# Kernel tuning notes

Hardware: AMD Instinct MI355X
Metric: run time of the kernel (lower is better)

Reference implementation:

```python
import jax, jax.numpy as jnp
import numpy as np

N, E, B, L = 20000, 320000, 64, 4
DIN_SEQ, DIN_STR, HID = 1280, 128, 256
NHEAD, HDIM = 8, 32
EPS = 1e-5
SLOPE = 0.2


def setup_inputs() -> dict:
    key = jax.random.key(0)
    ks = iter(jax.random.split(key, 64))
    def nrm(shape, scale=0.05):
        return jax.random.normal(next(ks), shape, dtype=jnp.float32) * scale
    return {
        "seq_x": jax.random.normal(next(ks), (N, DIN_SEQ), dtype=jnp.float32),
        "struct_x": jax.random.normal(next(ks), (N, DIN_STR), dtype=jnp.float32),
        "seq_edge_index": jax.random.randint(next(ks), (2, E), 0, N),
        "struct_edge_index": jax.random.randint(next(ks), (2, E), 0, N),
        "seq_batch": jnp.sort(jax.random.randint(next(ks), (N,), 0, B)),
        "struct_batch": jnp.sort(jax.random.randint(next(ks), (N,), 0, B)),
        "seq_proj_W": nrm((DIN_SEQ, HID)), "seq_proj_b": nrm((HID,)),
        "gcn_W": nrm((L, HID, HID)), "gcn_b": nrm((L, HID)),
        "seq_bn_g": jnp.ones((L, HID), jnp.float32), "seq_bn_b": jnp.zeros((L, HID), jnp.float32),
        "struct_proj_W": nrm((DIN_STR, HID)), "struct_proj_b": nrm((HID,)),
        "gat_W": nrm((L, HID, HID)), "gat_att_src": nrm((L, NHEAD, HDIM)),
        "gat_att_dst": nrm((L, NHEAD, HDIM)), "gat_b": nrm((L, HID)),
        "struct_bn_g": jnp.ones((L, HID), jnp.float32), "struct_bn_b": jnp.zeros((L, HID), jnp.float32),
        "Wq": nrm((HID, HID)), "bq": nrm((HID,)),
        "Wk": nrm((HID, HID)), "bk": nrm((HID,)),
        "Wv": nrm((HID, HID)), "bv": nrm((HID,)),
        "Wo": nrm((HID, HID)), "bo": nrm((HID,)),
        "fus_W": nrm((2 * HID, HID)), "fus_b": nrm((HID,)),
        "p1_W": nrm((HID, HID // 2)), "p1_b": nrm((HID // 2,)),
        "p2_W": nrm((HID // 2, 1)), "p2_b": nrm((1,)),
    }


def _add_self_loops(edge_index, n):
    loops = jnp.arange(n, dtype=edge_index.dtype)
    return jnp.concatenate([edge_index[0], loops]), jnp.concatenate([edge_index[1], loops])


def _batchnorm(x, g, b):
    # PyG BatchNorm forward (training-mode batch stats, biased variance, eps=1e-5)
    mu = x.mean(axis=0)
    var = x.var(axis=0)
    return g * (x - mu) * jax.lax.rsqrt(var + EPS) + b


def _gcn(x, src, dst, W, b):
    # GCNConv: symmetric-normalized gather -> scatter-add, self loops already appended
    n = x.shape[0]
    deg = jax.ops.segment_sum(jnp.ones_like(src, dtype=x.dtype), dst, num_segments=n)
    dinv = jax.lax.rsqrt(jnp.maximum(deg, 1.0))
    h = x @ W
    msg = h[src] * (dinv[src] * dinv[dst])[:, None]
    return jax.ops.segment_sum(msg, dst, num_segments=n) + b


def _seg_softmax(e, dst, n):
    m = jax.ops.segment_max(e, dst, num_segments=n)
    ex = jnp.exp(e - m[dst])
    s = jax.ops.segment_sum(ex, dst, num_segments=n)
    return ex / s[dst]


def _gat(x, src, dst, W, a_src, a_dst, b):
    # GATConv: per-edge LeakyReLU attention, softmax over incoming edges, concat heads
    n = x.shape[0]
    h = (x @ W).reshape(n, NHEAD, HDIM)
    e = jax.nn.leaky_relu((h * a_src).sum(-1)[src] + (h * a_dst).sum(-1)[dst], SLOPE)  # [E,H]
    alpha = _seg_softmax(e, dst, n)
    out = jax.ops.segment_sum(h[src] * alpha[:, :, None], dst, num_segments=n)
    return out.reshape(n, NHEAD * HDIM) + b


def _mean_pool(x, batch, nb):
    s = jax.ops.segment_sum(x, batch, num_segments=nb)
    c = jax.ops.segment_sum(jnp.ones((x.shape[0],), x.dtype), batch, num_segments=nb)
    return s / jnp.maximum(c, 1.0)[:, None]


def reference(seq_x, struct_x, seq_edge_index, struct_edge_index, seq_batch, struct_batch,
              seq_proj_W, seq_proj_b, gcn_W, gcn_b, seq_bn_g, seq_bn_b,
              struct_proj_W, struct_proj_b, gat_W, gat_att_src, gat_att_dst, gat_b,
              struct_bn_g, struct_bn_b, Wq, bq, Wk, bk, Wv, bv, Wo, bo,
              fus_W, fus_b, p1_W, p1_b, p2_W, p2_b):
    s_src, s_dst = _add_self_loops(seq_edge_index, seq_x.shape[0])
    t_src, t_dst = _add_self_loops(struct_edge_index, struct_x.shape[0])
    # sequence branch: GCN stack
    xs = jax.nn.relu(seq_x @ seq_proj_W + seq_proj_b)
    for l in range(gcn_W.shape[0]):
        xs = jax.nn.relu(_batchnorm(_gcn(xs, s_src, s_dst, gcn_W[l], gcn_b[l]), seq_bn_g[l], seq_bn_b[l]))
    xs = _mean_pool(xs, seq_batch, B)  # [B, HID]
    # structure branch: GAT stack
    xt = jax.nn.relu(struct_x @ struct_proj_W + struct_proj_b)
    for l in range(gat_W.shape[0]):
        xt = jax.nn.relu(_batchnorm(_gat(xt, t_src, t_dst, gat_W[l], gat_att_src[l], gat_att_dst[l], gat_b[l]), struct_bn_g[l], struct_bn_b[l]))
    xt = _mean_pool(xt, struct_batch, B)  # [B, HID]
    # cross-attention with query/key/value seq-len 1 (softmax over singleton axis)
    q = (xs @ Wq + bq).reshape(B, NHEAD, HDIM)
    k = (xt @ Wk + bk).reshape(B, NHEAD, HDIM)
    v = (xt @ Wv + bv).reshape(B, NHEAD, HDIM)
    scores = (q * k).sum(-1, keepdims=True) * (1.0 / np.sqrt(HDIM))  # [B,H,1]
    attn = jax.nn.softmax(scores, axis=-1)
    x_attn = (attn * v).reshape(B, HID) @ Wo + bo
    # fusion + predictor (dropout inactive at inference)
    xf = jax.nn.relu(jnp.concatenate([x_attn, xt], axis=1) @ fus_W + fus_b)
    h = jax.nn.relu(xf @ p1_W + p1_b)
    return h @ p2_W + p2_b  # [B, 1]
```

## Files before the change

### kernel.cpp

```cpp
#include <hip/hip_runtime.h>
#include <math.h>

#define NN 20000
#define NE 320000
#define NTOT (NE + NN)
#define NBATCH 64
#define HIDW 256
#define NHEADS 8
#define HD 32
#define NL 4
#define BEPS 1e-5f
#define LSLOPE 0.2f
#define WELEMS (128 * HIDW + NL * HIDW * HIDW)

typedef __attribute__((ext_vector_type(8))) short s16x8;
typedef __attribute__((ext_vector_type(8))) unsigned short u16x8;
typedef __attribute__((ext_vector_type(4))) float f32x4;

static __device__ __forceinline__ ushort f2bf(float f) {
  uint u = __float_as_uint(f);
  uint r = (u + 0x7fff + ((u >> 16) & 1)) >> 16;
  return (ushort)r;
}
static __device__ __forceinline__ float bf2f(ushort h) {
  return __uint_as_float(((uint)h) << 16);
}

__global__ __launch_bounds__(1024) void k_scan(const int* __restrict__ cnt,
                                               int* __restrict__ rowptr) {
  __shared__ int tsum[1024];
  int tid = threadIdx.x;
  const int per = (NN + 1023) / 1024;
  int start = tid * per;
  int local = 0;
  for (int j = 0; j < per; ++j) {
    int idx = start + j;
    if (idx < NN) local += cnt[idx];
  }
  tsum[tid] = local;
  __syncthreads();
  for (int off = 1; off < 1024; off <<= 1) {
    int v = (tid >= off) ? tsum[tid - off] : 0;
    __syncthreads();
    tsum[tid] += v;
    __syncthreads();
  }
  int run = (tid == 0) ? 0 : tsum[tid - 1];
  for (int j = 0; j < per; ++j) {
    int idx = start + j;
    if (idx < NN) { rowptr[idx] = run; run += cnt[idx]; }
  }
  if (tid == 1023) rowptr[NN] = tsum[1023];
}

__global__ void k_fill(const int* __restrict__ src, const int* __restrict__ dst,
                       const int* __restrict__ rowptr, int* __restrict__ cur,
                       int* __restrict__ srcs) {
  int i = blockIdx.x * blockDim.x + threadIdx.x;
  if (i >= NTOT) return;
  int s = (i < NE) ? src[i] : (i - NE);
  int d = (i < NE) ? dst[i] : (i - NE);
  int pos = rowptr[d] + atomicAdd(&cur[d], 1);
  srcs[pos] = s;
}

#define WB ((WELEMS + 255) / 256)
#define XB ((NN * 128 / 4 + 255) / 256)
#define HB ((NTOT + 255) / 256)
__global__ __launch_bounds__(256) void k_prep(const float* __restrict__ projW,
                                              const float* __restrict__ gatW,
                                              const float* __restrict__ sx,
                                              const int* __restrict__ e_dst,
                                              ushort* __restrict__ wh,
                                              ushort* __restrict__ wl,
                                              ushort* __restrict__ sxh,
                                              ushort* __restrict__ sxl,
                                              int* __restrict__ cnt) {
  int bb = blockIdx.x;
  if (bb < WB) {
    int i = bb * 256 + threadIdx.x;
    if (i >= WELEMS) return;
    float v;
    if (i < 128 * HIDW) {
      int n = i >> 7, k = i & 127;
      v = projW[k * HIDW + n];
    } else {
      int j = i - 128 * HIDW;
      int l = j >> 16, r = j & 65535;
      int n = r >> 8, k = r & 255;
      v = gatW[l * 65536 + k * HIDW + n];
    }
    ushort h = f2bf(v);
    wh[i] = h;
    wl[i] = f2bf(v - bf2f(h));
  } else if (bb < WB + XB) {
    int idx = (bb - WB) * 256 + threadIdx.x;
    if (idx >= NN * 128 / 4) return;
    int i0 = idx * 4;
    float4 v = *reinterpret_cast<const float4*>(&sx[i0]);
    float vv[4] = {v.x, v.y, v.z, v.w};
    ushort4 hh, ll;
    ushort h0 = f2bf(vv[0]); hh.x = h0; ll.x = f2bf(vv[0] - bf2f(h0));
    ushort h1 = f2bf(vv[1]); hh.y = h1; ll.y = f2bf(vv[1] - bf2f(h1));
    ushort h2 = f2bf(vv[2]); hh.z = h2; ll.z = f2bf(vv[2] - bf2f(h2));
    ushort h3 = f2bf(vv[3]); hh.w = h3; ll.w = f2bf(vv[3] - bf2f(h3));
    *reinterpret_cast<ushort4*>(&sxh[i0]) = hh;
    *reinterpret_cast<ushort4*>(&sxl[i0]) = ll;
  } else {
    int i = (bb - WB - XB) * 256 + threadIdx.x;
    if (i >= NTOT) return;
    int d = (i < NE) ? e_dst[i] : (i - NE);
    atomicAdd(&cnt[d], 1);
  }
}

__global__ __launch_bounds__(256) void k_asplit(const ushort* __restrict__ X,
                                                const float* __restrict__ stats,
                                                const float* __restrict__ g,
                                                const float* __restrict__ b,
                                                ushort* __restrict__ ah,
                                                ushort* __restrict__ al) {
  int idx = blockIdx.x * 256 + threadIdx.x;
  if (idx >= NN * HIDW / 8) return;
  int i0 = idx * 8;
  u16x8 xin = *reinterpret_cast<const u16x8*>(&X[i0]);
  int c = i0 & 255;
  u16x8 hh, ll;
#pragma unroll
  for (int j = 0; j < 8; ++j) {
    int cc = c + j;
    float mean = stats[cc] * (1.f / NN);
    float var = fmaxf(stats[HIDW + cc] * (1.f / NN) - mean * mean, 0.f);
    float sc = g[cc] * rsqrtf(var + BEPS);
    float sh = b[cc] - mean * sc;
    float v = fmaxf(bf2f(xin[j]) * sc + sh, 0.f);
    ushort h = f2bf(v);
    hh[j] = h;
    ll[j] = f2bf(v - bf2f(h));
  }
  *reinterpret_cast<u16x8*>(&ah[i0]) = hh;
  *reinterpret_cast<u16x8*>(&al[i0]) = ll;
}

#define GBM 64
#define GBN 64
#define GBK 64
#define NWG 1252
#define SWZ_Q 156
#define SWZ_R 4
__global__ __launch_bounds__(256) void k_mfma(const ushort* __restrict__ Ah,
                                              const ushort* __restrict__ Al,
                                              const ushort* __restrict__ Wh,
                                              const ushort* __restrict__ Wl,
                                              const float* __restrict__ bias,
                                              const float* __restrict__ aS,
                                              const float* __restrict__ aD,
                                              ushort* __restrict__ Coh,
                                              ushort* __restrict__ Col,
                                              ushort* __restrict__ Ch,
                                              float* __restrict__ asrc,
                                              float* __restrict__ adst,
                                              int M, int K, int mode) {
  __shared__ __align__(16) ushort As[2][GBM][72];
  __shared__ __align__(16) ushort Ws[2][GBN][72];
  int orig = blockIdx.x;
  int xcd = orig & 7, pos = orig >> 3;
  int wgid = (xcd < SWZ_R ? xcd * (SWZ_Q + 1) : SWZ_R * (SWZ_Q + 1) + (xcd - SWZ_R) * SWZ_Q) + pos;
  int rowblk = wgid >> 2, colblk = wgid & 3;
  int row0 = rowblk * GBM, col0 = colblk * GBN;

  int tid = threadIdx.x;
  int wid = tid >> 6, lane = tid & 63;
  int wr = wid >> 1, wc = wid & 1;
  int l15 = lane & 15, l4 = lane >> 4;
  f32x4 acc[2][2] = {};
  int sr = tid >> 2;
  int skq = (tid & 3) * 16;

  for (int k0 = 0; k0 < K; k0 += GBK) {
    int gr = row0 + sr;
    u16x8 vh0 = {0,0,0,0,0,0,0,0}, vh1 = vh0, vl0 = vh0, vl1 = vh0;
    if (gr < M) {
      vh0 = *reinterpret_cast<const u16x8*>(&Ah[(size_t)gr * K + k0 + skq]);
      vh1 = *reinterpret_cast<const u16x8*>(&Ah[(size_t)gr * K + k0 + skq + 8]);
      vl0 = *reinterpret_cast<const u16x8*>(&Al[(size_t)gr * K + k0 + skq]);
      vl1 = *reinterpret_cast<const u16x8*>(&Al[(size_t)gr * K + k0 + skq + 8]);
    }
    u16x8 wh0 = *reinterpret_cast<const u16x8*>(&Wh[(size_t)(col0 + sr) * K + k0 + skq]);
    u16x8 wh1 = *reinterpret_cast<const u16x8*>(&Wh[(size_t)(col0 + sr) * K + k0 + skq + 8]);
    u16x8 wl0 = *reinterpret_cast<const u16x8*>(&Wl[(size_t)(col0 + sr) * K + k0 + skq]);
    u16x8 wl1 = *reinterpret_cast<const u16x8*>(&Wl[(size_t)(col0 + sr) * K + k0 + skq + 8]);
    *reinterpret_cast<u16x8*>(&As[0][sr][skq]) = vh0;
    *reinterpret_cast<u16x8*>(&As[0][sr][skq + 8]) = vh1;
    *reinterpret_cast<u16x8*>(&As[1][sr][skq]) = vl0;
    *reinterpret_cast<u16x8*>(&As[1][sr][skq + 8]) = vl1;
    *reinterpret_cast<u16x8*>(&Ws[0][sr][skq]) = wh0;
    *reinterpret_cast<u16x8*>(&Ws[0][sr][skq + 8]) = wh1;
    *reinterpret_cast<u16x8*>(&Ws[1][sr][skq]) = wl0;
    *reinterpret_cast<u16x8*>(&Ws[1][sr][skq + 8]) = wl1;
    __syncthreads();

#pragma unroll
    for (int ks = 0; ks < 2; ++ks) {
      int ak = ks * 32 + l4 * 8;
      s16x8 af[2][2], bfv[2][2];
#pragma unroll
      for (int mf = 0; mf < 2; ++mf) {
        int ar = wr * 32 + mf * 16 + l15;
        af[mf][0] = *reinterpret_cast<const s16x8*>(&As[0][ar][ak]);
        af[mf][1] = *reinterpret_cast<const s16x8*>(&As[1][ar][ak]);
      }
#pragma unroll
      for (int nf = 0; nf < 2; ++nf) {
        int bn = wc * 32 + nf * 16 + l15;
        bfv[nf][0] = *reinterpret_cast<const s16x8*>(&Ws[0][bn][ak]);
        bfv[nf][1] = *reinterpret_cast<const s16x8*>(&Ws[1][bn][ak]);
      }
#pragma unroll
      for (int mf = 0; mf < 2; ++mf)
#pragma unroll
        for (int nf = 0; nf < 2; ++nf) {
          acc[mf][nf] = __builtin_amdgcn_mfma_f32_16x16x32_bf16(af[mf][0], bfv[nf][0], acc[mf][nf], 0, 0, 0);
          acc[mf][nf] = __builtin_amdgcn_mfma_f32_16x16x32_bf16(af[mf][0], bfv[nf][1], acc[mf][nf], 0, 0, 0);
          acc[mf][nf] = __builtin_amdgcn_mfma_f32_16x16x32_bf16(af[mf][1], bfv[nf][0], acc[mf][nf], 0, 0, 0);
        }
    }
    __syncthreads();
  }

  if (mode == 0) {
#pragma unroll
    for (int mf = 0; mf < 2; ++mf)
#pragma unroll
      for (int reg = 0; reg < 4; ++reg) {
        int r = row0 + wr * 32 + mf * 16 + l4 * 4 + reg;
        if (r >= M) continue;
#pragma unroll
        for (int nf = 0; nf < 2; ++nf) {
          int c = col0 + wc * 32 + nf * 16 + l15;
          float v = fmaxf(acc[mf][nf][reg] + bias[c], 0.f);
          ushort h = f2bf(v);
          Coh[(size_t)r * HIDW + c] = h;
          Col[(size_t)r * HIDW + c] = f2bf(v - bf2f(h));
        }
      }
  } else {
    int hg = colblk * 2 + wc;
    float aSv[2], aDv[2];
#pragma unroll
    for (int nf = 0; nf < 2; ++nf) {
      aSv[nf] = aS[hg * HD + nf * 16 + l15];
      aDv[nf] = aD[hg * HD + nf * 16 + l15];
    }
#pragma unroll
    for (int mf = 0; mf < 2; ++mf)
#pragma unroll
      for (int reg = 0; reg < 4; ++reg) {
        int r = row0 + wr * 32 + mf * 16 + l4 * 4 + reg;
        bool ok = (r < M);
        float pa = 0.f, pd = 0.f;
#pragma unroll
        for (int nf = 0; nf < 2; ++nf) {
          float v = acc[mf][nf][reg];
          if (ok) {
            int c = col0 + wc * 32 + nf * 16 + l15;
            Ch[(size_t)r * HIDW + c] = f2bf(v);
          }
          pa += v * aSv[nf];
          pd += v * aDv[nf];
        }
        pa += __shfl_xor(pa, 1); pa += __shfl_xor(pa, 2);
        pa += __shfl_xor(pa, 4); pa += __shfl_xor(pa, 8);
        pd += __shfl_xor(pd, 1); pd += __shfl_xor(pd, 2);
        pd += __shfl_xor(pd, 4); pd += __shfl_xor(pd, 8);
        if (ok && l15 == 0) {
          asrc[r * NHEADS + hg] = pa;
          adst[r * NHEADS + hg] = pd;
        }
      }
  }
}

__global__ __launch_bounds__(256) void k_agg(const ushort* __restrict__ h,
                                             const int* __restrict__ rowptr,
                                             const int* __restrict__ srcs,
                                             const float* __restrict__ asrc,
                                             const float* __restrict__ adst,
                                             ushort* __restrict__ out,
                                             float* __restrict__ stats64) {
  __shared__ float sst[4][512];
  int tid = threadIdx.x;
  int wid = tid >> 6, lane = tid & 63;
  int node = blockIdx.x * 4 + wid;
  int el = lane >> 5, sl = lane & 31;
  int c0 = sl * 8, hh = sl >> 2;
  float adn = adst[node * NHEADS + hh];
  int beg = rowptr[node], end = rowptr[node + 1];
  int deg = end - beg;
  float acc[8] = {};
  float ssum = 0.f;
  for (int w0 = 0; w0 < deg; w0 += 64) {
    int sv = srcs[min(beg + w0 + lane, end - 1)];
    int lim = min(64, deg - w0);
    for (int cb = 0; cb < lim; cb += 16) {
      int s[8];
#pragma unroll
      for (int j = 0; j < 8; ++j) s[j] = __shfl(sv, cb + 2 * j + el);
      float a[8];
      u16x8 hv[8];
#pragma unroll
      for (int j = 0; j < 8; ++j) {
        a[j] = asrc[s[j] * NHEADS + hh];
        hv[j] = *reinterpret_cast<const u16x8*>(&h[(size_t)s[j] * HIDW + c0]);
      }
#pragma unroll
      for (int j = 0; j < 8; ++j) {
        float e = a[j] + adn;
        e = (e >= 0.f) ? e : LSLOPE * e;
        float ex = ((cb + 2 * j + el) < lim) ? __expf(e) : 0.f;
        ssum += ex;
#pragma unroll
        for (int q = 0; q < 8; ++q) acc[q] += ex * bf2f(hv[j][q]);
      }
    }
  }
  ssum += __shfl_xor(ssum, 32);
#pragma unroll
  for (int q = 0; q < 8; ++q) acc[q] += __shfl_xor(acc[q], 32);
  if (el == 0) {
    float inv = 1.f / ssum;
    u16x8 o;
    float of[8];
#pragma unroll
    for (int q = 0; q < 8; ++q) {
      of[q] = acc[q] * inv;
      o[q] = f2bf(of[q]);
    }
    *reinterpret_cast<u16x8*>(&out[(size_t)node * HIDW + c0]) = o;
#pragma unroll
    for (int q = 0; q < 8; ++q) {
      sst[wid][c0 + q] = of[q];
      sst[wid][256 + c0 + q] = of[q] * of[q];
    }
  }
  __syncthreads();
  int c = tid;
  float s = sst[0][c] + sst[1][c] + sst[2][c] + sst[3][c];
  float s2 = sst[0][256 + c] + sst[1][256 + c] + sst[2][256 + c] + sst[3][256 + c];
  float* slice = stats64 + (size_t)(blockIdx.x & 63) * 512;
  atomicAdd(&slice[c], s);
  atomicAdd(&slice[256 + c], s2);
}

__global__ __launch_bounds__(512) void k_red(const float* __restrict__ stats64,
                                             float* __restrict__ stats) {
  int c = threadIdx.x;
  float s = 0.f;
  for (int i = 0; i < 64; ++i) s += stats64[(size_t)i * 512 + c];
  stats[c] = s;
}

__global__ __launch_bounds__(256) void k_pool(const ushort* __restrict__ x,
                                              const float* __restrict__ stats64,
                                              const float* __restrict__ g,
                                              const float* __restrict__ b,
                                              const int* __restrict__ batch,
                                              float* __restrict__ pool,
                                              int* __restrict__ pcnt) {
  int c = threadIdx.x;
  float st = 0.f, st2 = 0.f;
  for (int i = 0; i < 64; ++i) {
    st += stats64[(size_t)i * 512 + c];
    st2 += stats64[(size_t)i * 512 + 256 + c];
  }
  float mean = st * (1.f / NN);
  float var = fmaxf(st2 * (1.f / NN) - mean * mean, 0.f);
  float sc = g[c] * rsqrtf(var + BEPS);
  float sh = b[c] - mean * sc;
  const int RPB = (NN + 255) / 256;
  int r0 = blockIdx.x * RPB, r1 = min(r0 + RPB, NN);
  if (r0 >= r1) return;
  int curb = batch[r0];
  float acc = 0.f;
  int run = 0;
  for (int r = r0; r < r1; ++r) {
    int bb = batch[r];
    if (bb != curb) {
      atomicAdd(&pool[curb * HIDW + c], acc);
      if (c == 0) atomicAdd(&pcnt[curb], run);
      acc = 0.f; run = 0; curb = bb;
    }
    float v = fmaxf(bf2f(x[(size_t)r * HIDW + c]) * sc + sh, 0.f);
    acc += v;
    run++;
  }
  atomicAdd(&pool[curb * HIDW + c], acc);
  if (c == 0) atomicAdd(&pcnt[curb], run);
}

__global__ __launch_bounds__(256) void k_head(const float* __restrict__ pool,
                                              const int* __restrict__ pcnt,
                                              const float* __restrict__ Wv, const float* __restrict__ bv,
                                              const float* __restrict__ Wo, const float* __restrict__ bo,
                                              const float* __restrict__ fusW, const float* __restrict__ fusB,
                                              const float* __restrict__ p1W, const float* __restrict__ p1b,
                                              const float* __restrict__ p2W, const float* __restrict__ p2b,
                                              float* __restrict__ out) {
  __shared__ float pr[HIDW], sA[HIDW], sB[HIDW], sH[128];
  int b = blockIdx.x, c = threadIdx.x;
  float invc = 1.f / fmaxf((float)pcnt[b], 1.f);
  pr[c] = pool[b * HIDW + c] * invc;
  __syncthreads();
  float acc = bv[c];
  for (int k = 0; k < HIDW; ++k) acc += pr[k] * Wv[k * HIDW + c];
  sA[c] = acc;
  __syncthreads();
  acc = bo[c];
  for (int k = 0; k < HIDW; ++k) acc += sA[k] * Wo[k * HIDW + c];
  sB[c] = acc;
  __syncthreads();
  acc = fusB[c];
  for (int k = 0; k < HIDW; ++k) acc += sB[k] * fusW[k * HIDW + c];
  for (int k = 0; k < HIDW; ++k) acc += pr[k] * fusW[(HIDW + k) * HIDW + c];
  float xf = fmaxf(acc, 0.f);
  __syncthreads();
  sA[c] = xf;
  __syncthreads();
  if (c < 128) {
    acc = p1b[c];
    for (int k = 0; k < HIDW; ++k) acc += sA[k] * p1W[k * 128 + c];
    sH[c] = fmaxf(acc, 0.f);
  }
  __syncthreads();
  if (c == 0) {
    float s = p2b[0];
    for (int k = 0; k < 128; ++k) s += sH[k] * p2W[k];
    out[b] = s;
  }
}

extern "C" void kernel_launch(void* const* d_in, const int* in_sizes, int n_in,
                              void* d_out, int out_size, void* d_ws, size_t ws_size,
                              hipStream_t stream) {
  const float* struct_x = (const float*)d_in[1];
  const int* edge = (const int*)d_in[3];
  const int* batch = (const int*)d_in[5];
  const float* projW = (const float*)d_in[12];
  const float* projB = (const float*)d_in[13];
  const float* gatW = (const float*)d_in[14];
  const float* attS = (const float*)d_in[15];
  const float* attD = (const float*)d_in[16];
  const float* bnG = (const float*)d_in[18];
  const float* bnB = (const float*)d_in[19];
  const float* Wv = (const float*)d_in[24];
  const float* bv = (const float*)d_in[25];
  const float* Wo = (const float*)d_in[26];
  const float* bo = (const float*)d_in[27];
  const float* fusW = (const float*)d_in[28];
  const float* fusB = (const float*)d_in[29];
  const float* p1W = (const float*)d_in[30];
  const float* p1b = (const float*)d_in[31];
  const float* p2W = (const float*)d_in[32];
  const float* p2b = (const float*)d_in[33];
  float* out = (float*)d_out;

  const int* e_src = edge;
  const int* e_dst = edge + NE;

  char* ws = (char*)d_ws;
  size_t off = 0;
  auto alloc = [&](size_t bytes) -> void* {
    void* p = ws + off;
    off = (off + bytes + 255) & ~(size_t)255;
    return p;
  };
  ushort* buf0 = (ushort*)alloc((size_t)NN * HIDW * 2);
  ushort* hb = (ushort*)alloc((size_t)NN * HIDW * 2);
  ushort* a0h = (ushort*)alloc((size_t)NN * HIDW * 2);
  ushort* a0l = (ushort*)alloc((size_t)NN * HIDW * 2);
  ushort* sxh = (ushort*)alloc((size_t)NN * 128 * 2);
  ushort* sxl = (ushort*)alloc((size_t)NN * 128 * 2);
  ushort* wth = (ushort*)alloc((size_t)WELEMS * 2);
  ushort* wtl = (ushort*)alloc((size_t)WELEMS * 2);
  int* rowptr = (int*)alloc((NN + 1) * 4);
  int* srcs = (int*)alloc((size_t)NTOT * 4);
  float* asrc = (float*)alloc((size_t)NN * NHEADS * 4);
  float* adst = (float*)alloc((size_t)NN * NHEADS * 4);
  float* stats = (float*)alloc(NL * 512 * 4);
  char* zero_base = ws + off;
  int* cnt = (int*)alloc(NN * 4);
  int* cur = (int*)alloc(NN * 4);
  float* stats64 = (float*)alloc((size_t)NL * 64 * 512 * 4);
  float* pool = (float*)alloc(NBATCH * HIDW * 4);
  int* pcnt = (int*)alloc(NBATCH * 4);
  size_t zero_bytes = (ws + off) - zero_base;

  const int TPB = 256;
  const int gEdge = (NTOT + TPB - 1) / TPB;

  hipMemsetAsync(zero_base, 0, zero_bytes, stream);

  k_prep<<<WB + XB + HB, TPB, 0, stream>>>(projW, gatW, struct_x, e_dst,
                                           wth, wtl, sxh, sxl, cnt);
  k_scan<<<1, 1024, 0, stream>>>(cnt, rowptr);
  k_fill<<<gEdge, TPB, 0, stream>>>(e_src, e_dst, rowptr, cur, srcs);

  k_mfma<<<NWG, 256, 0, stream>>>(sxh, sxl, wth, wtl, projB, nullptr, nullptr,
                                  a0h, a0l, nullptr, nullptr, nullptr, NN, 128, 0);

  for (int l = 0; l < NL; ++l) {
    const ushort* whL = wth + 128 * HIDW + (size_t)l * HIDW * HIDW;
    const ushort* wlL = wtl + 128 * HIDW + (size_t)l * HIDW * HIDW;
    float* s64 = stats64 + (size_t)l * 64 * 512;
    k_mfma<<<NWG, 256, 0, stream>>>(a0h, a0l, whL, wlL, nullptr,
                                    attS + l * HIDW, attD + l * HIDW,
                                    nullptr, nullptr, hb, asrc, adst, NN, HIDW, 1);
    k_agg<<<NN / 4, 256, 0, stream>>>(hb, rowptr, srcs, asrc, adst, buf0, s64);
    if (l < NL - 1) {
      k_red<<<1, 512, 0, stream>>>(s64, stats + l * 512);
      k_asplit<<<(NN * HIDW / 8 + TPB - 1) / TPB, TPB, 0, stream>>>(
          buf0, stats + l * 512, bnG + l * HIDW, bnB + l * HIDW, a0h, a0l);
    }
  }

  k_pool<<<256, 256, 0, stream>>>(buf0, stats64 + (size_t)3 * 64 * 512,
                                  bnG + 3 * HIDW, bnB + 3 * HIDW, batch, pool, pcnt);

  k_head<<<NBATCH, 256, 0, stream>>>(pool, pcnt, Wv, bv, Wo, bo, fusW, fusB,
                                     p1W, p1b, p2W, p2b, out);
}
```

Before: 359.9 us.

## Drop bf16 hi/lo split GEMM to single bf16 and fuse stat reduction into BN-apply

```diff
diff --git a/kernel.cpp b/kernel.cpp
--- a/kernel.cpp
+++ b/kernel.cpp
@@ -72,9 +72,7 @@
                                               const float* __restrict__ sx,
                                               const int* __restrict__ e_dst,
                                               ushort* __restrict__ wh,
-                                              ushort* __restrict__ wl,
                                               ushort* __restrict__ sxh,
-                                              ushort* __restrict__ sxl,
                                               int* __restrict__ cnt) {
   int bb = blockIdx.x;
   if (bb < WB) {
@@ -90,22 +88,15 @@
       int n = r >> 8, k = r & 255;
       v = gatW[l * 65536 + k * HIDW + n];
     }
-    ushort h = f2bf(v);
-    wh[i] = h;
-    wl[i] = f2bf(v - bf2f(h));
+    wh[i] = f2bf(v);
   } else if (bb < WB + XB) {
     int idx = (bb - WB) * 256 + threadIdx.x;
     if (idx >= NN * 128 / 4) return;
     int i0 = idx * 4;
     float4 v = *reinterpret_cast<const float4*>(&sx[i0]);
-    float vv[4] = {v.x, v.y, v.z, v.w};
-    ushort4 hh, ll;
-    ushort h0 = f2bf(vv[0]); hh.x = h0; ll.x = f2bf(vv[0] - bf2f(h0));
-    ushort h1 = f2bf(vv[1]); hh.y = h1; ll.y = f2bf(vv[1] - bf2f(h1));
-    ushort h2 = f2bf(vv[2]); hh.z = h2; ll.z = f2bf(vv[2] - bf2f(h2));
-    ushort h3 = f2bf(vv[3]); hh.w = h3; ll.w = f2bf(vv[3] - bf2f(h3));
+    ushort4 hh;
+    hh.x = f2bf(v.x); hh.y = f2bf(v.y); hh.z = f2bf(v.z); hh.w = f2bf(v.w);
     *reinterpret_cast<ushort4*>(&sxh[i0]) = hh;
-    *reinterpret_cast<ushort4*>(&sxl[i0]) = ll;
   } else {
     int i = (bb - WB - XB) * 256 + threadIdx.x;
     if (i >= NTOT) return;
@@ -114,32 +105,39 @@
   }
 }
 
+#define ARPB 79
 __global__ __launch_bounds__(256) void k_asplit(const ushort* __restrict__ X,
-                                                const float* __restrict__ stats,
+                                                const float* __restrict__ stats64,
                                                 const float* __restrict__ g,
                                                 const float* __restrict__ b,
-                                                ushort* __restrict__ ah,
-                                                ushort* __restrict__ al) {
-  int idx = blockIdx.x * 256 + threadIdx.x;
-  if (idx >= NN * HIDW / 8) return;
-  int i0 = idx * 8;
-  u16x8 xin = *reinterpret_cast<const u16x8*>(&X[i0]);
-  int c = i0 & 255;
-  u16x8 hh, ll;
-#pragma unroll
-  for (int j = 0; j < 8; ++j) {
-    int cc = c + j;
-    float mean = stats[cc] * (1.f / NN);
-    float var = fmaxf(stats[HIDW + cc] * (1.f / NN) - mean * mean, 0.f);
-    float sc = g[cc] * rsqrtf(var + BEPS);
-    float sh = b[cc] - mean * sc;
-    float v = fmaxf(bf2f(xin[j]) * sc + sh, 0.f);
-    ushort h = f2bf(v);
-    hh[j] = h;
-    ll[j] = f2bf(v - bf2f(h));
-  }
-  *reinterpret_cast<u16x8*>(&ah[i0]) = hh;
-  *reinterpret_cast<u16x8*>(&al[i0]) = ll;
+                                                ushort* __restrict__ ah) {
+  __shared__ float sc_s[HIDW], sh_s[HIDW];
+  int c = threadIdx.x;
+  float st = 0.f, st2 = 0.f;
+  for (int i = 0; i < 64; ++i) {
+    st += stats64[(size_t)i * 512 + c];
+    st2 += stats64[(size_t)i * 512 + 256 + c];
+  }
+  float mean = st * (1.f / NN);
+  float var = fmaxf(st2 * (1.f / NN) - mean * mean, 0.f);
+  float sc = g[c] * rsqrtf(var + BEPS);
+  sc_s[c] = sc;
+  sh_s[c] = b[c] - mean * sc;
+  __syncthreads();
+  int r0 = blockIdx.x * ARPB, r1 = min(r0 + ARPB, NN);
+  int ch = (c & 31) * 8;
+  for (int rb = r0; rb < r1; rb += 8) {
+    int r = rb + (c >> 5);
+    if (r >= r1) continue;
+    u16x8 xin = *reinterpret_cast<const u16x8*>(&X[(size_t)r * HIDW + ch]);
+    u16x8 hh;
+#pragma unroll
+    for (int j = 0; j < 8; ++j) {
+      float v = fmaxf(bf2f(xin[j]) * sc_s[ch + j] + sh_s[ch + j], 0.f);
+      hh[j] = f2bf(v);
+    }
+    *reinterpret_cast<u16x8*>(&ah[(size_t)r * HIDW + ch]) = hh;
+  }
 }
 
 #define GBM 64
@@ -149,20 +147,17 @@
 #define SWZ_Q 156
 #define SWZ_R 4
 __global__ __launch_bounds__(256) void k_mfma(const ushort* __restrict__ Ah,
-                                              const ushort* __restrict__ Al,
                                               const ushort* __restrict__ Wh,
-                                              const ushort* __restrict__ Wl,
                                               const float* __restrict__ bias,
                                               const float* __restrict__ aS,
                                               const float* __restrict__ aD,
-                                              ushort* __restrict__ Coh,
-                                              ushort* __restrict__ Col,
+                                              ushort* __restrict__ Co,
                                               ushort* __restrict__ Ch,
                                               float* __restrict__ asrc,
                                               float* __restrict__ adst,
                                               int M, int K, int mode) {
-  __shared__ __align__(16) ushort As[2][GBM][72];
-  __shared__ __align__(16) ushort Ws[2][GBN][72];
+  __shared__ __align__(16) ushort As[GBM][72];
+  __shared__ __align__(16) ushort Ws[GBN][72];
   int orig = blockIdx.x;
   int xcd = orig & 7, pos = orig >> 3;
   int wgid = (xcd < SWZ_R ? xcd * (SWZ_Q + 1) : SWZ_R * (SWZ_Q + 1) + (xcd - SWZ_R) * SWZ_Q) + pos;
@@ -179,51 +174,34 @@
 
   for (int k0 = 0; k0 < K; k0 += GBK) {
     int gr = row0 + sr;
-    u16x8 vh0 = {0,0,0,0,0,0,0,0}, vh1 = vh0, vl0 = vh0, vl1 = vh0;
+    u16x8 va0 = {0,0,0,0,0,0,0,0}, va1 = va0;
     if (gr < M) {
-      vh0 = *reinterpret_cast<const u16x8*>(&Ah[(size_t)gr * K + k0 + skq]);
-      vh1 = *reinterpret_cast<const u16x8*>(&Ah[(size_t)gr * K + k0 + skq + 8]);
-      vl0 = *reinterpret_cast<const u16x8*>(&Al[(size_t)gr * K + k0 + skq]);
-      vl1 = *reinterpret_cast<const u16x8*>(&Al[(size_t)gr * K + k0 + skq + 8]);
-    }
-    u16x8 wh0 = *reinterpret_cast<const u16x8*>(&Wh[(size_t)(col0 + sr) * K + k0 + skq]);
-    u16x8 wh1 = *reinterpret_cast<const u16x8*>(&Wh[(size_t)(col0 + sr) * K + k0 + skq + 8]);
-    u16x8 wl0 = *reinterpret_cast<const u16x8*>(&Wl[(size_t)(col0 + sr) * K + k0 + skq]);
-    u16x8 wl1 = *reinterpret_cast<const u16x8*>(&Wl[(size_t)(col0 + sr) * K + k0 + skq + 8]);
-    *reinterpret_cast<u16x8*>(&As[0][sr][skq]) = vh0;
-    *reinterpret_cast<u16x8*>(&As[0][sr][skq + 8]) = vh1;
-    *reinterpret_cast<u16x8*>(&As[1][sr][skq]) = vl0;
-    *reinterpret_cast<u16x8*>(&As[1][sr][skq + 8]) = vl1;
-    *reinterpret_cast<u16x8*>(&Ws[0][sr][skq]) = wh0;
-    *reinterpret_cast<u16x8*>(&Ws[0][sr][skq + 8]) = wh1;
-    *reinterpret_cast<u16x8*>(&Ws[1][sr][skq]) = wl0;
-    *reinterpret_cast<u16x8*>(&Ws[1][sr][skq + 8]) = wl1;
+      va0 = *reinterpret_cast<const u16x8*>(&Ah[(size_t)gr * K + k0 + skq]);
+      va1 = *reinterpret_cast<const u16x8*>(&Ah[(size_t)gr * K + k0 + skq + 8]);
+    }
+    u16x8 vw0 = *reinterpret_cast<const u16x8*>(&Wh[(size_t)(col0 + sr) * K + k0 + skq]);
+    u16x8 vw1 = *reinterpret_cast<const u16x8*>(&Wh[(size_t)(col0 + sr) * K + k0 + skq + 8]);
+    *reinterpret_cast<u16x8*>(&As[sr][skq]) = va0;
+    *reinterpret_cast<u16x8*>(&As[sr][skq + 8]) = va1;
+    *reinterpret_cast<u16x8*>(&Ws[sr][skq]) = vw0;
+    *reinterpret_cast<u16x8*>(&Ws[sr][skq + 8]) = vw1;
     __syncthreads();
 
 #pragma unroll
     for (int ks = 0; ks < 2; ++ks) {
       int ak = ks * 32 + l4 * 8;
-      s16x8 af[2][2], bfv[2][2];
-#pragma unroll
-      for (int mf = 0; mf < 2; ++mf) {
-        int ar = wr * 32 + mf * 16 + l15;
-        af[mf][0] = *reinterpret_cast<const s16x8*>(&As[0][ar][ak]);
-        af[mf][1] = *reinterpret_cast<const s16x8*>(&As[1][ar][ak]);
-      }
-#pragma unroll
-      for (int nf = 0; nf < 2; ++nf) {
-        int bn = wc * 32 + nf * 16 + l15;
-        bfv[nf][0] = *reinterpret_cast<const s16x8*>(&Ws[0][bn][ak]);
-        bfv[nf][1] = *reinterpret_cast<const s16x8*>(&Ws[1][bn][ak]);
-      }
+      s16x8 af[2], bfv[2];
 #pragma unroll
       for (int mf = 0; mf < 2; ++mf)
-#pragma unroll
-        for (int nf = 0; nf < 2; ++nf) {
-          acc[mf][nf] = __builtin_amdgcn_mfma_f32_16x16x32_bf16(af[mf][0], bfv[nf][0], acc[mf][nf], 0, 0, 0);
-          acc[mf][nf] = __builtin_amdgcn_mfma_f32_16x16x32_bf16(af[mf][0], bfv[nf][1], acc[mf][nf], 0, 0, 0);
-          acc[mf][nf] = __builtin_amdgcn_mfma_f32_16x16x32_bf16(af[mf][1], bfv[nf][0], acc[mf][nf], 0, 0, 0);
-        }
+        af[mf] = *reinterpret_cast<const s16x8*>(&As[wr * 32 + mf * 16 + l15][ak]);
+#pragma unroll
+      for (int nf = 0; nf < 2; ++nf)
+        bfv[nf] = *reinterpret_cast<const s16x8*>(&Ws[wc * 32 + nf * 16 + l15][ak]);
+#pragma unroll
+      for (int mf = 0; mf < 2; ++mf)
+#pragma unroll
+        for (int nf = 0; nf < 2; ++nf)
+          acc[mf][nf] = __builtin_amdgcn_mfma_f32_16x16x32_bf16(af[mf], bfv[nf], acc[mf][nf], 0, 0, 0);
     }
     __syncthreads();
   }
@@ -239,9 +217,7 @@
         for (int nf = 0; nf < 2; ++nf) {
           int c = col0 + wc * 32 + nf * 16 + l15;
           float v = fmaxf(acc[mf][nf][reg] + bias[c], 0.f);
-          ushort h = f2bf(v);
-          Coh[(size_t)r * HIDW + c] = h;
-          Col[(size_t)r * HIDW + c] = f2bf(v - bf2f(h));
+          Co[(size_t)r * HIDW + c] = f2bf(v);
         }
       }
   } else {
@@ -350,14 +326,6 @@
   float* slice = stats64 + (size_t)(blockIdx.x & 63) * 512;
   atomicAdd(&slice[c], s);
   atomicAdd(&slice[256 + c], s2);
-}
-
-__global__ __launch_bounds__(512) void k_red(const float* __restrict__ stats64,
-                                             float* __restrict__ stats) {
-  int c = threadIdx.x;
-  float s = 0.f;
-  for (int i = 0; i < 64; ++i) s += stats64[(size_t)i * 512 + c];
-  stats[c] = s;
 }
 
 __global__ __launch_bounds__(256) void k_pool(const ushort* __restrict__ x,
@@ -476,17 +444,13 @@
   };
   ushort* buf0 = (ushort*)alloc((size_t)NN * HIDW * 2);
   ushort* hb = (ushort*)alloc((size_t)NN * HIDW * 2);
-  ushort* a0h = (ushort*)alloc((size_t)NN * HIDW * 2);
-  ushort* a0l = (ushort*)alloc((size_t)NN * HIDW * 2);
+  ushort* a0 = (ushort*)alloc((size_t)NN * HIDW * 2);
   ushort* sxh = (ushort*)alloc((size_t)NN * 128 * 2);
-  ushort* sxl = (ushort*)alloc((size_t)NN * 128 * 2);
   ushort* wth = (ushort*)alloc((size_t)WELEMS * 2);
-  ushort* wtl = (ushort*)alloc((size_t)WELEMS * 2);
   int* rowptr = (int*)alloc((NN + 1) * 4);
   int* srcs = (int*)alloc((size_t)NTOT * 4);
   float* asrc = (float*)alloc((size_t)NN * NHEADS * 4);
   float* adst = (float*)alloc((size_t)NN * NHEADS * 4);
-  float* stats = (float*)alloc(NL * 512 * 4);
   char* zero_base = ws + off;
   int* cnt = (int*)alloc(NN * 4);
   int* cur = (int*)alloc(NN * 4);
@@ -500,26 +464,23 @@
 
   hipMemsetAsync(zero_base, 0, zero_bytes, stream);
 
-  k_prep<<<WB + XB + HB, TPB, 0, stream>>>(projW, gatW, struct_x, e_dst,
-                                           wth, wtl, sxh, sxl, cnt);
+  k_prep<<<WB + XB + HB, TPB, 0, stream>>>(projW, gatW, struct_x, e_dst, wth, sxh, cnt);
   k_scan<<<1, 1024, 0, stream>>>(cnt, rowptr);
   k_fill<<<gEdge, TPB, 0, stream>>>(e_src, e_dst, rowptr, cur, srcs);
 
-  k_mfma<<<NWG, 256, 0, stream>>>(sxh, sxl, wth, wtl, projB, nullptr, nullptr,
-                                  a0h, a0l, nullptr, nullptr, nullptr, NN, 128, 0);
+  k_mfma<<<NWG, 256, 0, stream>>>(sxh, wth, projB, nullptr, nullptr,
+                                  a0, nullptr, nullptr, nullptr, NN, 128, 0);
 
   for (int l = 0; l < NL; ++l) {
     const ushort* whL = wth + 128 * HIDW + (size_t)l * HIDW * HIDW;
-    const ushort* wlL = wtl + 128 * HIDW + (size_t)l * HIDW * HIDW;
     float* s64 = stats64 + (size_t)l * 64 * 512;
-    k_mfma<<<NWG, 256, 0, stream>>>(a0h, a0l, whL, wlL, nullptr,
+    k_mfma<<<NWG, 256, 0, stream>>>(a0, whL, nullptr,
                                     attS + l * HIDW, attD + l * HIDW,
-                                    nullptr, nullptr, hb, asrc, adst, NN, HIDW, 1);
+                                    nullptr, hb, asrc, adst, NN, HIDW, 1);
     k_agg<<<NN / 4, 256, 0, stream>>>(hb, rowptr, srcs, asrc, adst, buf0, s64);
     if (l < NL - 1) {
-      k_red<<<1, 512, 0, stream>>>(s64, stats + l * 512);
-      k_asplit<<<(NN * HIDW / 8 + TPB - 1) / TPB, TPB, 0, stream>>>(
-          buf0, stats + l * 512, bnG + l * HIDW, bnB + l * HIDW, a0h, a0l);
+      k_asplit<<<(NN + ARPB - 1) / ARPB, TPB, 0, stream>>>(
+          buf0, s64, bnG + l * HIDW, bnB + l * HIDW, a0);
     }
   }
 
```

Measured after the change: 333.1 us. -7.4%, faster.
